# Optimization experiments

Hardware: AMD Instinct MI355X
Metric: run time of the kernel (lower is better)

Reference implementation:

```python
import jax, jax.numpy as jnp
import numpy as np

TEMP = 0.05          # self.temp
NUM_LABELED = 15080  # SysuDataset bank size


def setup_inputs() -> dict:
    key = jax.random.key(0)
    k1, k2, k3, k4, k5 = jax.random.split(key, 5)
    B, D, L = 512, 2048, NUM_LABELED
    f = jax.random.normal(k1, (B, D), jnp.float32)
    features = f / jnp.linalg.norm(f, axis=1, keepdims=True)  # L2-normalized embeddings
    fk = jax.random.normal(k2, (B, D), jnp.float32)
    features_k = fk / jnp.linalg.norm(fk, axis=1, keepdims=True)
    gt_labels = jax.random.randint(k3, (B, 5), 0, L)   # last column = pid index
    gt_labels_k = jax.random.randint(k4, (B, 5), 0, L)
    bank = jax.random.normal(k5, (L, D), jnp.float32)
    bank_features = bank / jnp.linalg.norm(bank, axis=1, keepdims=True)
    return {"features": features, "features_k": features_k,
            "gt_labels": gt_labels, "gt_labels_k": gt_labels_k,
            "bank_features": bank_features}


def reference(features, features_k, gt_labels, gt_labels_k, bank_features):
    # pids = cat([i[:, -1] for i in gt_labels]); all >= 0 by construction, so the
    # pids > -1 filter is an identity (static shapes under jit).
    pids = gt_labels[:, -1]                                  # [B]
    # HM.forward: inputs.mm(features.t()), then /= temp
    sim_all = (features @ bank_features.T) / TEMP            # [B, L]
    # segment-mean of logits grouped by memory label (labels == arange -> identity,
    # kept for faithfulness to the index_add / nums normalization in the source)
    labels = jnp.arange(NUM_LABELED)
    sim = jax.ops.segment_sum(sim_all.T, labels, num_segments=NUM_LABELED)  # [L, B]
    nums = jax.ops.segment_sum(jnp.ones((NUM_LABELED, 1), jnp.float32),
                               labels, num_segments=NUM_LABELED)            # [L, 1]
    sim = sim / nums
    logits = sim.T                                           # [B, L]
    logp = jax.nn.log_softmax(logits, axis=-1)
    loss = -jnp.mean(jnp.take_along_axis(logp, pids[:, None], axis=1))
    return loss
```

## Files before the change

kernel.cpp:

```cpp
#include <hip/hip_runtime.h>
#include <hip/hip_bf16.h>

#define M_ROWS 512
#define N_COLS 15080
#define K_DIM  2048
#define BM 128
#define BN 128
#define BKF 64
#define NT 118
#define KSTEPS 32
#define SCALE 20.0f

#define BANK_PAD_ROWS 15104
#define BANK_PAD_E (30932992ull)
#define FEAT_E     (1048576ull)
#define NG_CVT     (3997696ull)

typedef _Float16 f16x8 __attribute__((ext_vector_type(8)));
typedef float    f32x4 __attribute__((ext_vector_type(4)));

#define GLD_LDS16(gp, lp) __builtin_amdgcn_global_load_lds( \
    (const __attribute__((address_space(1))) void*)(gp),    \
    (__attribute__((address_space(3))) void*)(lp), 16, 0, 0)

extern "C" __global__ __launch_bounds__(256)
void k_cvt(const float* __restrict__ feat, const float* __restrict__ bank,
           _Float16* __restrict__ out)
{
    const size_t stride = (size_t)gridDim.x * 256;
    for (size_t g = (size_t)blockIdx.x * 256 + threadIdx.x; g < NG_CVT; g += stride) {
        const size_t e = g * 8;
        f16x8 h;
        if (e < BANK_PAD_E) {
            const int row = (int)(e >> 11);
            if (row < N_COLS) {
                const float4 x = *(const float4*)(bank + e);
                const float4 y = *(const float4*)(bank + e + 4);
                h[0] = (_Float16)x.x; h[1] = (_Float16)x.y; h[2] = (_Float16)x.z; h[3] = (_Float16)x.w;
                h[4] = (_Float16)y.x; h[5] = (_Float16)y.y; h[6] = (_Float16)y.z; h[7] = (_Float16)y.w;
            } else {
                h = (f16x8)(_Float16)0.0f;
            }
        } else {
            const size_t e2 = e - BANK_PAD_E;
            const float4 x = *(const float4*)(feat + e2);
            const float4 y = *(const float4*)(feat + e2 + 4);
            h[0] = (_Float16)x.x; h[1] = (_Float16)x.y; h[2] = (_Float16)x.z; h[3] = (_Float16)x.w;
            h[4] = (_Float16)y.x; h[5] = (_Float16)y.y; h[6] = (_Float16)y.z; h[7] = (_Float16)y.w;
        }
        *(f16x8*)(out + e) = h;
    }
}

extern "C" __global__ __launch_bounds__(256, 2)
void k_gemm16(const _Float16* __restrict__ A16,
              const _Float16* __restrict__ B16,
              const int*      __restrict__ gt,
              float* __restrict__ pm,
              float* __restrict__ ps,
              float* __restrict__ tv)
{
    __shared__ __align__(16) char lds[65536];

    const int t  = threadIdx.x;
    const int bx = blockIdx.x;

    int mi, nt;
    if (bx < 448) { const int slot = bx & 7; const int rest = bx >> 3;
                    mi = rest & 3; nt = (rest >> 2) * 8 + slot; }
    else          { const int r2 = bx - 448; mi = r2 & 3; nt = 112 + (r2 >> 2); }
    const int rowA0 = mi * BM;
    const int rowB0 = nt * BN;

    const int lane = t & 63, w = t >> 6;
    const int lr = lane >> 3, gg = lane & 7;
    const size_t aE0 = (size_t)(rowA0 + w * 32 + lr) * K_DIM + (size_t)((gg ^ lr) * 8);
    const size_t bE0 = (size_t)(rowB0 + w * 32 + lr) * K_DIM + (size_t)((gg ^ lr) * 8);
    const char* aP0 = (const char*)(A16 + aE0);
    const char* bP0 = (const char*)(B16 + bE0);
    const int ldsW = w * 4096;

    auto STAGE = [&](int kt, int sel) {
        const int   dofs = sel * 32768;
        const size_t ko  = (size_t)kt * 128;
#pragma unroll
        for (int j = 0; j < 4; j++) {
            GLD_LDS16(aP0 + (size_t)j * 32768 + ko, lds + dofs + ldsW + j * 1024);
            GLD_LDS16(bP0 + (size_t)j * 32768 + ko, lds + dofs + 16384 + ldsW + j * 1024);
        }
    };

    const int wm = w >> 1, wn = w & 1;
    const int q = lane >> 4, r = lane & 15;
    int aaddr[4][2], baddr[4][2];
#pragma unroll
    for (int m = 0; m < 4; m++) {
        const int rowa = wm * 64 + m * 16 + r;
        const int rowb = wn * 64 + m * 16 + r;
#pragma unroll
        for (int ks = 0; ks < 2; ks++) {
            aaddr[m][ks] = (rowa * 128 + ks * 64 + q * 16) ^ ((rowa & 7) << 4);
            baddr[m][ks] = 16384 + ((rowb * 128 + ks * 64 + q * 16) ^ ((rowb & 7) << 4));
        }
    }

    f32x4 acc[4][4];
    const f32x4 zero = {0.f, 0.f, 0.f, 0.f};
#pragma unroll
    for (int m = 0; m < 4; m++)
#pragma unroll
        for (int n = 0; n < 4; n++) acc[m][n] = zero;

    auto COMPUTE = [&](int sel) {
        const char* bb = lds + sel * 32768;
        f16x8 bf[4][2];
#pragma unroll
        for (int n = 0; n < 4; n++)
#pragma unroll
            for (int ks = 0; ks < 2; ks++)
                bf[n][ks] = *(const f16x8*)(bb + baddr[n][ks]);
#pragma unroll
        for (int m = 0; m < 4; m++) {
            const f16x8 af0 = *(const f16x8*)(bb + aaddr[m][0]);
            const f16x8 af1 = *(const f16x8*)(bb + aaddr[m][1]);
#pragma unroll
            for (int n = 0; n < 4; n++) {
                acc[m][n] = __builtin_amdgcn_mfma_f32_16x16x32_f16(af0, bf[n][0], acc[m][n], 0, 0, 0);
                acc[m][n] = __builtin_amdgcn_mfma_f32_16x16x32_f16(af1, bf[n][1], acc[m][n], 0, 0, 0);
            }
        }
    };

    STAGE(0, 0);
    __syncthreads();
#pragma unroll 2
    for (int kt = 0; kt < KSTEPS - 1; kt++) {
        STAGE(kt + 1, (kt + 1) & 1);
        COMPUTE(kt & 1);
        __syncthreads();
    }
    COMPUTE((KSTEPS - 1) & 1);

    __syncthreads();
    float* redm = (float*)lds;
    float* reds = ((float*)lds) + 256;

#pragma unroll
    for (int m = 0; m < 4; m++) {
#pragma unroll
        for (int j = 0; j < 4; j++) {
            const int lrow = wm * 64 + m * 16 + q * 4 + j;
            const int grow = rowA0 + lrow;
            const int pid  = gt[grow * 5 + 4];
            float sv[4];
            float mx = -INFINITY;
#pragma unroll
            for (int n = 0; n < 4; n++) {
                const int gc = rowB0 + wn * 64 + n * 16 + r;
                float s = SCALE * acc[m][n][j];
                s = (gc < N_COLS) ? s : -INFINITY;
                sv[n] = s;
                mx = fmaxf(mx, s);
                if (gc == pid) tv[grow] = s;
            }
#pragma unroll
            for (int d = 1; d < 16; d <<= 1) mx = fmaxf(mx, __shfl_xor(mx, d, 16));
            float se = 0.f;
#pragma unroll
            for (int n = 0; n < 4; n++) se += __expf(sv[n] - mx);
#pragma unroll
            for (int d = 1; d < 16; d <<= 1) se += __shfl_xor(se, d, 16);
            if (r == 0) { redm[wn * 128 + lrow] = mx; reds[wn * 128 + lrow] = se; }
        }
    }
    __syncthreads();
    if (t < 128) {
        const float m0 = redm[t], m1 = redm[128 + t];
        const float s0 = reds[t], s1 = reds[128 + t];
        const float Mv = fmaxf(m0, m1);
        const float Sv = s0 * __expf(m0 - Mv) + s1 * __expf(m1 - Mv);
        pm[(rowA0 + t) * NT + nt] = Mv;
        ps[(rowA0 + t) * NT + nt] = Sv;
    }
}

extern "C" __global__ __launch_bounds__(128)
void k_rowlse(const float* __restrict__ pm,
              const float* __restrict__ ps,
              const float* __restrict__ tv,
              float* __restrict__ rowloss)
{
    const int b = blockIdx.x;
    const int i = threadIdx.x;
    __shared__ float wred[4];

    const float m = (i < NT) ? pm[b * NT + i] : -INFINITY;
    const float s = (i < NT) ? ps[b * NT + i] : 0.f;

    float M = m;
#pragma unroll
    for (int d = 1; d < 64; d <<= 1) M = fmaxf(M, __shfl_xor(M, d, 64));
    if ((i & 63) == 0) wred[i >> 6] = M;
    __syncthreads();
    M = fmaxf(wred[0], wred[1]);
    __syncthreads();

    float e = (i < NT) ? s * __expf(m - M) : 0.f;
#pragma unroll
    for (int d = 1; d < 64; d <<= 1) e += __shfl_xor(e, d, 64);
    if ((i & 63) == 0) wred[i >> 6] = e;
    __syncthreads();
    if (i == 0) {
        const float S = wred[0] + wred[1];
        rowloss[b] = M + logf(S) - tv[b];
    }
}

extern "C" __global__ __launch_bounds__(512)
void k_final(const float* __restrict__ rowloss, float* __restrict__ out)
{
    __shared__ float red[512];
    const int b = threadIdx.x;
    red[b] = rowloss[b];
    __syncthreads();
    for (int s = 256; s > 0; s >>= 1) {
        if (b < s) red[b] += red[b + s];
        __syncthreads();
    }
    if (b == 0) out[0] = red[0] / 512.0f;
}

extern "C" __global__ __launch_bounds__(512, 4)
void k_gemm_lse(const float* __restrict__ A,
                const float* __restrict__ Bk,
                const int*   __restrict__ gt,
                float* __restrict__ pm, float* __restrict__ ps,
                float* __restrict__ tv)
{
    __shared__ __align__(16) ushort lds[16384];
    const int t  = threadIdx.x;
    const int bx = blockIdx.x;
    int mi, nt;
    if (bx < 448) { const int slot = bx & 7; const int rest = bx >> 3;
                    mi = rest & 3; nt = (rest >> 2) * 8 + slot; }
    else          { const int r2 = bx - 448; mi = r2 & 3; nt = 112 + (r2 >> 2); }
    const int rowA0 = mi * BM, rowB0 = nt * BN;

    int arow[2], ag[2];
#pragma unroll
    for (int i = 0; i < 2; i++) { int G = t + i * 512; arow[i] = G >> 3; ag[i] = G & 7; }
    float4 ra[4], rb[4];
    auto LOAD = [&](int kt) {
#pragma unroll
        for (int i = 0; i < 2; i++) {
            const float* pa = A + (size_t)(rowA0 + arow[i]) * K_DIM + kt * BKF + ag[i] * 8;
            ra[2*i] = *(const float4*)(pa); ra[2*i+1] = *(const float4*)(pa + 4);
            const int br = rowB0 + arow[i];
            if (br < N_COLS) {
                const float* pb = Bk + (size_t)br * K_DIM + kt * BKF + ag[i] * 8;
                rb[2*i] = *(const float4*)(pb); rb[2*i+1] = *(const float4*)(pb + 4);
            } else { rb[2*i] = make_float4(0,0,0,0); rb[2*i+1] = make_float4(0,0,0,0); }
        }
    };
    auto STORE = [&]() {
#pragma unroll
        for (int i = 0; i < 2; i++) {
            const int ba = (arow[i] * 128 + ag[i] * 16) ^ ((arow[i] & 7) << 4);
            f16x8 ha, hb;
            float4 x = ra[2*i], y = ra[2*i+1];
            ha[0]=(_Float16)x.x; ha[1]=(_Float16)x.y; ha[2]=(_Float16)x.z; ha[3]=(_Float16)x.w;
            ha[4]=(_Float16)y.x; ha[5]=(_Float16)y.y; ha[6]=(_Float16)y.z; ha[7]=(_Float16)y.w;
            x = rb[2*i]; y = rb[2*i+1];
            hb[0]=(_Float16)x.x; hb[1]=(_Float16)x.y; hb[2]=(_Float16)x.z; hb[3]=(_Float16)x.w;
            hb[4]=(_Float16)y.x; hb[5]=(_Float16)y.y; hb[6]=(_Float16)y.z; hb[7]=(_Float16)y.w;
            *(f16x8*)((char*)lds + ba) = ha;
            *(f16x8*)((char*)lds + 16384 + ba) = hb;
        }
    };
    const int lane = t & 63, wid = t >> 6;
    const int wm = wid >> 2, wn = wid & 3;
    const int q = lane >> 4, r = lane & 15;
    int aaddr[4][2], baddr[2][2];
#pragma unroll
    for (int m = 0; m < 4; m++) { const int rowa = wm*64 + m*16 + r;
#pragma unroll
        for (int ks = 0; ks < 2; ks++) aaddr[m][ks] = (rowa*128 + ks*64 + q*16) ^ ((rowa&7)<<4); }
#pragma unroll
    for (int n = 0; n < 2; n++) { const int rowb = wn*32 + n*16 + r;
#pragma unroll
        for (int ks = 0; ks < 2; ks++) baddr[n][ks] = 16384 + ((rowb*128 + ks*64 + q*16) ^ ((rowb&7)<<4)); }

    f32x4 acc[4][2];
    const f32x4 zero = {0.f,0.f,0.f,0.f};
#pragma unroll
    for (int m = 0; m < 4; m++)
#pragma unroll
        for (int n = 0; n < 2; n++) acc[m][n] = zero;

    LOAD(0);
    for (int kt = 0; kt < KSTEPS; kt++) {
        __syncthreads(); STORE(); __syncthreads();
        if (kt + 1 < KSTEPS) LOAD(kt + 1);
        f16x8 bf[2][2];
#pragma unroll
        for (int n = 0; n < 2; n++)
#pragma unroll
            for (int ks = 0; ks < 2; ks++) bf[n][ks] = *(const f16x8*)((const char*)lds + baddr[n][ks]);
#pragma unroll
        for (int m = 0; m < 4; m++) {
            const f16x8 af0 = *(const f16x8*)((const char*)lds + aaddr[m][0]);
            const f16x8 af1 = *(const f16x8*)((const char*)lds + aaddr[m][1]);
#pragma unroll
            for (int n = 0; n < 2; n++) {
                acc[m][n] = __builtin_amdgcn_mfma_f32_16x16x32_f16(af0, bf[n][0], acc[m][n], 0,0,0);
                acc[m][n] = __builtin_amdgcn_mfma_f32_16x16x32_f16(af1, bf[n][1], acc[m][n], 0,0,0);
            }
        }
    }
    __syncthreads();
    float* redm = (float*)lds;
    float* reds = ((float*)lds) + 512;
#pragma unroll
    for (int m = 0; m < 4; m++) {
#pragma unroll
        for (int j = 0; j < 4; j++) {
            const int lrow = wm*64 + m*16 + q*4 + j;
            const int grow = rowA0 + lrow;
            const int pid  = gt[grow*5 + 4];
            float sv[2]; float mx = -INFINITY;
#pragma unroll
            for (int n = 0; n < 2; n++) {
                const int gc = rowB0 + wn*32 + n*16 + r;
                float s = SCALE * acc[m][n][j];
                s = (gc < N_COLS) ? s : -INFINITY;
                sv[n] = s; mx = fmaxf(mx, s);
                if (gc == pid) tv[grow] = s;
            }
#pragma unroll
            for (int d = 1; d < 16; d <<= 1) mx = fmaxf(mx, __shfl_xor(mx, d, 16));
            float se = 0.f;
#pragma unroll
            for (int n = 0; n < 2; n++) se += __expf(sv[n] - mx);
#pragma unroll
            for (int d = 1; d < 16; d <<= 1) se += __shfl_xor(se, d, 16);
            if (r == 0) { redm[wn*128 + lrow] = mx; reds[wn*128 + lrow] = se; }
        }
    }
    __syncthreads();
    if (t < 128) {
        float Mv = -INFINITY;
#pragma unroll
        for (int c = 0; c < 4; c++) Mv = fmaxf(Mv, redm[c*128 + t]);
        float Sv = 0.f;
#pragma unroll
        for (int c = 0; c < 4; c++) Sv += reds[c*128 + t] * __expf(redm[c*128 + t] - Mv);
        pm[(rowA0 + t) * NT + nt] = Mv;
        ps[(rowA0 + t) * NT + nt] = Sv;
    }
}

extern "C" void kernel_launch(void* const* d_in, const int* in_sizes, int n_in,
                              void* d_out, int out_size, void* d_ws, size_t ws_size,
                              hipStream_t stream)
{
    const float* feat = (const float*)d_in[0];
    const int*   gt   = (const int*)d_in[2];
    const float* bank = (const float*)d_in[4];

    const size_t NEED = (BANK_PAD_E + FEAT_E) * 2 + (size_t)512 * NT * 4 * 2 + 512 * 4 * 2;
    if (ws_size >= NEED) {
        _Float16* bank16 = (_Float16*)d_ws;
        _Float16* feat16 = bank16 + BANK_PAD_E;
        float* pm = (float*)(feat16 + FEAT_E);
        float* ps = pm + 512 * NT;
        float* tv = ps + 512 * NT;
        float* rl = tv + 512;
        k_cvt<<<dim3(2048), 256, 0, stream>>>(feat, bank, bank16);
        k_gemm16<<<dim3(4 * NT), 256, 0, stream>>>(feat16, bank16, gt, pm, ps, tv);
        k_rowlse<<<dim3(512), 128, 0, stream>>>(pm, ps, tv, rl);
        k_final<<<dim3(1), 512, 0, stream>>>(rl, (float*)d_out);
    } else {
        float* pm = (float*)d_ws;
        float* ps = pm + 512 * NT;
        float* tv = ps + 512 * NT;
        float* rl = tv + 512;
        k_gemm_lse<<<dim3(4 * NT), 512, 0, stream>>>(feat, bank, gt, pm, ps, tv);
        k_rowlse<<<dim3(512), 128, 0, stream>>>(pm, ps, tv, rl);
        k_final<<<dim3(1), 512, 0, stream>>>(rl, (float*)d_out);
    }
}
```

Baseline: 239.5 us.

## Deepen GEMM LDS pipeline to four stages with explicit vmcnt waits

Replaces the double-buffered global-to-LDS pipeline with a 4-slot ring buffer in dynamic shared memory (128 KB), prefetching three k-steps ahead. The blanket __syncthreads is replaced by counted s_waitcnt vmcnt plus s_barrier, so loads stay in flight across iterations and memory latency is hidden better. Launch bounds drop to one block per CU because of the larger LDS footprint, which trades occupancy for deeper prefetch. The hand-written wait counts must match the number of outstanding loads per stage or correctness breaks.

```diff
diff --git a/kernel.cpp b/kernel.cpp
--- a/kernel.cpp
+++ b/kernel.cpp
@@ -52,7 +52,7 @@
     }
 }
 
-extern "C" __global__ __launch_bounds__(256, 2)
+extern "C" __global__ __launch_bounds__(256, 1)
 void k_gemm16(const _Float16* __restrict__ A16,
               const _Float16* __restrict__ B16,
               const int*      __restrict__ gt,
@@ -60,7 +60,7 @@
               float* __restrict__ ps,
               float* __restrict__ tv)
 {
-    __shared__ __align__(16) char lds[65536];
+    extern __shared__ char lds[];
 
     const int t  = threadIdx.x;
     const int bx = blockIdx.x;
@@ -80,8 +80,8 @@
     const char* bP0 = (const char*)(B16 + bE0);
     const int ldsW = w * 4096;
 
-    auto STAGE = [&](int kt, int sel) {
-        const int   dofs = sel * 32768;
+    auto STAGE = [&](int kt) {
+        const int   dofs = (kt & 3) * 32768;
         const size_t ko  = (size_t)kt * 128;
 #pragma unroll
         for (int j = 0; j < 4; j++) {
@@ -111,8 +111,8 @@
 #pragma unroll
         for (int n = 0; n < 4; n++) acc[m][n] = zero;
 
-    auto COMPUTE = [&](int sel) {
-        const char* bb = lds + sel * 32768;
+    auto COMPUTE = [&](int kt) {
+        const char* bb = lds + (kt & 3) * 32768;
         f16x8 bf[4][2];
 #pragma unroll
         for (int n = 0; n < 4; n++)
@@ -131,15 +131,20 @@
         }
     };
 
-    STAGE(0, 0);
-    __syncthreads();
-#pragma unroll 2
-    for (int kt = 0; kt < KSTEPS - 1; kt++) {
-        STAGE(kt + 1, (kt + 1) & 1);
-        COMPUTE(kt & 1);
-        __syncthreads();
-    }
-    COMPUTE((KSTEPS - 1) & 1);
+    STAGE(0); STAGE(1); STAGE(2);
+    asm volatile("s_waitcnt vmcnt(16)" ::: "memory");
+    __builtin_amdgcn_s_barrier();
+
+    for (int kt = 0; kt < KSTEPS; kt++) {
+        if (kt + 3 < KSTEPS) STAGE(kt + 3);
+        COMPUTE(kt);
+        if (kt + 1 < KSTEPS) {
+            if (kt <= KSTEPS - 4)      asm volatile("s_waitcnt vmcnt(16)" ::: "memory");
+            else if (kt == KSTEPS - 3) asm volatile("s_waitcnt vmcnt(8)"  ::: "memory");
+            else                       asm volatile("s_waitcnt vmcnt(0)"  ::: "memory");
+            __builtin_amdgcn_s_barrier();
+        }
+    }
 
     __syncthreads();
     float* redm = (float*)lds;
@@ -376,7 +381,7 @@
         float* tv = ps + 512 * NT;
         float* rl = tv + 512;
         k_cvt<<<dim3(2048), 256, 0, stream>>>(feat, bank, bank16);
-        k_gemm16<<<dim3(4 * NT), 256, 0, stream>>>(feat16, bank16, gt, pm, ps, tv);
+        k_gemm16<<<dim3(4 * NT), 256, 131072, stream>>>(feat16, bank16, gt, pm, ps, tv);
         k_rowlse<<<dim3(512), 128, 0, stream>>>(pm, ps, tv, rl);
         k_final<<<dim3(1), 512, 0, stream>>>(rl, (float*)d_out);
     } else {
```

Result: slower. 258.6 us (+8.0%).

## Split-K the fp16 GEMM in two and move the softmax reduction to a separate pass

Applied to the files above, without the earlier changes.

The fp16 MFMA GEMM now splits K into two halves, doubling the workgroup count from 472 to 944 so more waves are in flight across the CUs. Each half writes its raw partial dot products to a full [2, 512, N_PAD] fp32 workspace, with an XCD-aware block remap. A new per-row kernel sums the two partials, scales them, and computes an online log-sum-exp plus the target logit. This replaces the fused in-epilogue max/sum reduction. In exchange it adds roughly 62 MB of extra global writes and reads for the partial logits.

```diff
diff --git a/kernel.cpp b/kernel.cpp
--- a/kernel.cpp
+++ b/kernel.cpp
@@ -3,15 +3,18 @@
 
 #define M_ROWS 512
 #define N_COLS 15080
+#define N_PAD  15104
 #define K_DIM  2048
 #define BM 128
 #define BN 128
-#define BKF 64
 #define NT 118
 #define KSTEPS 32
 #define SCALE 20.0f
 
-#define BANK_PAD_ROWS 15104
+#define KS 2
+#define KSLICE 1024
+#define KSTEPS_SK 16
+
 #define BANK_PAD_E (30932992ull)
 #define FEAT_E     (1048576ull)
 #define NG_CVT     (3997696ull)
@@ -53,29 +56,28 @@
 }
 
 extern "C" __global__ __launch_bounds__(256, 2)
-void k_gemm16(const _Float16* __restrict__ A16,
-              const _Float16* __restrict__ B16,
-              const int*      __restrict__ gt,
-              float* __restrict__ pm,
-              float* __restrict__ ps,
-              float* __restrict__ tv)
+void k_gemm16sk(const _Float16* __restrict__ A16,
+                const _Float16* __restrict__ B16,
+                float* __restrict__ part)
 {
     __shared__ __align__(16) char lds[65536];
 
     const int t  = threadIdx.x;
     const int bx = blockIdx.x;
 
-    int mi, nt;
-    if (bx < 448) { const int slot = bx & 7; const int rest = bx >> 3;
-                    mi = rest & 3; nt = (rest >> 2) * 8 + slot; }
-    else          { const int r2 = bx - 448; mi = r2 & 3; nt = 112 + (r2 >> 2); }
+    const int wgid = (bx & 7) * 118 + (bx >> 3);
+    const int mi = wgid & 3;
+    const int ks = (wgid >> 2) & 1;
+    const int nt = wgid >> 3;
     const int rowA0 = mi * BM;
     const int rowB0 = nt * BN;
+    float* outp = part + (size_t)ks * M_ROWS * N_PAD;
 
     const int lane = t & 63, w = t >> 6;
     const int lr = lane >> 3, gg = lane & 7;
-    const size_t aE0 = (size_t)(rowA0 + w * 32 + lr) * K_DIM + (size_t)((gg ^ lr) * 8);
-    const size_t bE0 = (size_t)(rowB0 + w * 32 + lr) * K_DIM + (size_t)((gg ^ lr) * 8);
+    const size_t kbase = (size_t)ks * KSLICE;
+    const size_t aE0 = (size_t)(rowA0 + w * 32 + lr) * K_DIM + kbase + (size_t)((gg ^ lr) * 8);
+    const size_t bE0 = (size_t)(rowB0 + w * 32 + lr) * K_DIM + kbase + (size_t)((gg ^ lr) * 8);
     const char* aP0 = (const char*)(A16 + aE0);
     const char* bP0 = (const char*)(B16 + bE0);
     const int ldsW = w * 4096;
@@ -98,9 +100,9 @@
         const int rowa = wm * 64 + m * 16 + r;
         const int rowb = wn * 64 + m * 16 + r;
 #pragma unroll
-        for (int ks = 0; ks < 2; ks++) {
-            aaddr[m][ks] = (rowa * 128 + ks * 64 + q * 16) ^ ((rowa & 7) << 4);
-            baddr[m][ks] = 16384 + ((rowb * 128 + ks * 64 + q * 16) ^ ((rowb & 7) << 4));
+        for (int k2 = 0; k2 < 2; k2++) {
+            aaddr[m][k2] = (rowa * 128 + k2 * 64 + q * 16) ^ ((rowa & 7) << 4);
+            baddr[m][k2] = 16384 + ((rowb * 128 + k2 * 64 + q * 16) ^ ((rowb & 7) << 4));
         }
     }
 
@@ -117,8 +119,8 @@
 #pragma unroll
         for (int n = 0; n < 4; n++)
 #pragma unroll
-            for (int ks = 0; ks < 2; ks++)
-                bf[n][ks] = *(const f16x8*)(bb + baddr[n][ks]);
+            for (int k2 = 0; k2 < 2; k2++)
+                bf[n][k2] = *(const f16x8*)(bb + baddr[n][k2]);
 #pragma unroll
         for (int m = 0; m < 4; m++) {
             const f16x8 af0 = *(const f16x8*)(bb + aaddr[m][0]);
@@ -134,85 +136,66 @@
     STAGE(0, 0);
     __syncthreads();
 #pragma unroll 2
-    for (int kt = 0; kt < KSTEPS - 1; kt++) {
+    for (int kt = 0; kt < KSTEPS_SK - 1; kt++) {
         STAGE(kt + 1, (kt + 1) & 1);
         COMPUTE(kt & 1);
         __syncthreads();
     }
-    COMPUTE((KSTEPS - 1) & 1);
-
-    __syncthreads();
-    float* redm = (float*)lds;
-    float* reds = ((float*)lds) + 256;
-
-#pragma unroll
-    for (int m = 0; m < 4; m++) {
+    COMPUTE((KSTEPS_SK - 1) & 1);
+
+#pragma unroll
+    for (int m = 0; m < 4; m++)
 #pragma unroll
         for (int j = 0; j < 4; j++) {
-            const int lrow = wm * 64 + m * 16 + q * 4 + j;
-            const int grow = rowA0 + lrow;
-            const int pid  = gt[grow * 5 + 4];
-            float sv[4];
-            float mx = -INFINITY;
-#pragma unroll
-            for (int n = 0; n < 4; n++) {
-                const int gc = rowB0 + wn * 64 + n * 16 + r;
-                float s = SCALE * acc[m][n][j];
-                s = (gc < N_COLS) ? s : -INFINITY;
-                sv[n] = s;
-                mx = fmaxf(mx, s);
-                if (gc == pid) tv[grow] = s;
-            }
-#pragma unroll
-            for (int d = 1; d < 16; d <<= 1) mx = fmaxf(mx, __shfl_xor(mx, d, 16));
-            float se = 0.f;
-#pragma unroll
-            for (int n = 0; n < 4; n++) se += __expf(sv[n] - mx);
-#pragma unroll
-            for (int d = 1; d < 16; d <<= 1) se += __shfl_xor(se, d, 16);
-            if (r == 0) { redm[wn * 128 + lrow] = mx; reds[wn * 128 + lrow] = se; }
-        }
-    }
-    __syncthreads();
-    if (t < 128) {
-        const float m0 = redm[t], m1 = redm[128 + t];
-        const float s0 = reds[t], s1 = reds[128 + t];
-        const float Mv = fmaxf(m0, m1);
-        const float Sv = s0 * __expf(m0 - Mv) + s1 * __expf(m1 - Mv);
-        pm[(rowA0 + t) * NT + nt] = Mv;
-        ps[(rowA0 + t) * NT + nt] = Sv;
-    }
-}
-
-extern "C" __global__ __launch_bounds__(128)
-void k_rowlse(const float* __restrict__ pm,
-              const float* __restrict__ ps,
-              const float* __restrict__ tv,
-              float* __restrict__ rowloss)
+            const int grow = rowA0 + wm * 64 + m * 16 + q * 4 + j;
+            float* rowp = outp + (size_t)grow * N_PAD + rowB0 + wn * 64 + r;
+#pragma unroll
+            for (int n = 0; n < 4; n++) rowp[n * 16] = acc[m][n][j];
+        }
+}
+
+extern "C" __global__ __launch_bounds__(256)
+void k_lse(const float* __restrict__ part,
+           const int*   __restrict__ gt,
+           float* __restrict__ rowloss)
 {
     const int b = blockIdx.x;
-    const int i = threadIdx.x;
-    __shared__ float wred[4];
-
-    const float m = (i < NT) ? pm[b * NT + i] : -INFINITY;
-    const float s = (i < NT) ? ps[b * NT + i] : 0.f;
-
-    float M = m;
-#pragma unroll
-    for (int d = 1; d < 64; d <<= 1) M = fmaxf(M, __shfl_xor(M, d, 64));
-    if ((i & 63) == 0) wred[i >> 6] = M;
-    __syncthreads();
-    M = fmaxf(wred[0], wred[1]);
-    __syncthreads();
-
-    float e = (i < NT) ? s * __expf(m - M) : 0.f;
-#pragma unroll
-    for (int d = 1; d < 64; d <<= 1) e += __shfl_xor(e, d, 64);
-    if ((i & 63) == 0) wred[i >> 6] = e;
-    __syncthreads();
-    if (i == 0) {
-        const float S = wred[0] + wred[1];
-        rowloss[b] = M + logf(S) - tv[b];
+    const int t = threadIdx.x;
+    __shared__ float lm[4], ls[4];
+
+    const float4* p0 = (const float4*)(part + (size_t)b * N_PAD);
+    const float4* p1 = (const float4*)(part + (size_t)(M_ROWS + b) * N_PAD);
+
+    float m = -1e30f, s = 0.f;
+    for (int c = t; c < 3770; c += 256) {
+        const float4 a = p0[c], d = p1[c];
+        const float x0 = SCALE * (a.x + d.x);
+        const float x1 = SCALE * (a.y + d.y);
+        const float x2 = SCALE * (a.z + d.z);
+        const float x3 = SCALE * (a.w + d.w);
+        const float mx = fmaxf(fmaxf(x0, x1), fmaxf(x2, x3));
+        if (mx > m) { s *= __expf(m - mx); m = mx; }
+        s += __expf(x0 - m) + __expf(x1 - m) + __expf(x2 - m) + __expf(x3 - m);
+    }
+#pragma unroll
+    for (int d = 1; d < 64; d <<= 1) {
+        const float om = __shfl_xor(m, d, 64);
+        const float os = __shfl_xor(s, d, 64);
+        const float nm = fmaxf(m, om);
+        s = s * __expf(m - nm) + os * __expf(om - nm);
+        m = nm;
+    }
+    if ((t & 63) == 0) { lm[t >> 6] = m; ls[t >> 6] = s; }
+    __syncthreads();
+    if (t == 0) {
+        float M = fmaxf(fmaxf(lm[0], lm[1]), fmaxf(lm[2], lm[3]));
+        float S = 0.f;
+#pragma unroll
+        for (int w = 0; w < 4; w++) S += ls[w] * __expf(lm[w] - M);
+        const int pid = gt[b * 5 + 4];
+        const float tgt = SCALE * (part[(size_t)b * N_PAD + pid] +
+                                   part[(size_t)(M_ROWS + b) * N_PAD + pid]);
+        rowloss[b] = M + logf(S) - tgt;
     }
 }
 
@@ -253,11 +236,11 @@
     auto LOAD = [&](int kt) {
 #pragma unroll
         for (int i = 0; i < 2; i++) {
-            const float* pa = A + (size_t)(rowA0 + arow[i]) * K_DIM + kt * BKF + ag[i] * 8;
+            const float* pa = A + (size_t)(rowA0 + arow[i]) * K_DIM + kt * 64 + ag[i] * 8;
             ra[2*i] = *(const float4*)(pa); ra[2*i+1] = *(const float4*)(pa + 4);
             const int br = rowB0 + arow[i];
             if (br < N_COLS) {
-                const float* pb = Bk + (size_t)br * K_DIM + kt * BKF + ag[i] * 8;
+                const float* pb = Bk + (size_t)br * K_DIM + kt * 64 + ag[i] * 8;
                 rb[2*i] = *(const float4*)(pb); rb[2*i+1] = *(const float4*)(pb + 4);
             } else { rb[2*i] = make_float4(0,0,0,0); rb[2*i+1] = make_float4(0,0,0,0); }
         }
@@ -284,11 +267,11 @@
 #pragma unroll
     for (int m = 0; m < 4; m++) { const int rowa = wm*64 + m*16 + r;
 #pragma unroll
-        for (int ks = 0; ks < 2; ks++) aaddr[m][ks] = (rowa*128 + ks*64 + q*16) ^ ((rowa&7)<<4); }
+        for (int k2 = 0; k2 < 2; k2++) aaddr[m][k2] = (rowa*128 + k2*64 + q*16) ^ ((rowa&7)<<4); }
 #pragma unroll
     for (int n = 0; n < 2; n++) { const int rowb = wn*32 + n*16 + r;
 #pragma unroll
-        for (int ks = 0; ks < 2; ks++) baddr[n][ks] = 16384 + ((rowb*128 + ks*64 + q*16) ^ ((rowb&7)<<4)); }
+        for (int k2 = 0; k2 < 2; k2++) baddr[n][k2] = 16384 + ((rowb*128 + k2*64 + q*16) ^ ((rowb&7)<<4)); }
 
     f32x4 acc[4][2];
     const f32x4 zero = {0.f,0.f,0.f,0.f};
@@ -305,7 +288,7 @@
 #pragma unroll
         for (int n = 0; n < 2; n++)
 #pragma unroll
-            for (int ks = 0; ks < 2; ks++) bf[n][ks] = *(const f16x8*)((const char*)lds + baddr[n][ks]);
+            for (int k2 = 0; k2 < 2; k2++) bf[n][k2] = *(const f16x8*)((const char*)lds + baddr[n][k2]);
 #pragma unroll
         for (int m = 0; m < 4; m++) {
             const f16x8 af0 = *(const f16x8*)((const char*)lds + aaddr[m][0]);
@@ -359,6 +342,38 @@
     }
 }
 
+extern "C" __global__ __launch_bounds__(128)
+void k_rowlse(const float* __restrict__ pm,
+              const float* __restrict__ ps,
+              const float* __restrict__ tv,
+              float* __restrict__ rowloss)
+{
+    const int b = blockIdx.x;
+    const int i = threadIdx.x;
+    __shared__ float wred[4];
+
+    const float m = (i < NT) ? pm[b * NT + i] : -INFINITY;
+    const float s = (i < NT) ? ps[b * NT + i] : 0.f;
+
+    float M = m;
+#pragma unroll
+    for (int d = 1; d < 64; d <<= 1) M = fmaxf(M, __shfl_xor(M, d, 64));
+    if ((i & 63) == 0) wred[i >> 6] = M;
+    __syncthreads();
+    M = fmaxf(wred[0], wred[1]);
+    __syncthreads();
+
+    float e = (i < NT) ? s * __expf(m - M) : 0.f;
+#pragma unroll
+    for (int d = 1; d < 64; d <<= 1) e += __shfl_xor(e, d, 64);
+    if ((i & 63) == 0) wred[i >> 6] = e;
+    __syncthreads();
+    if (i == 0) {
+        const float S = wred[0] + wred[1];
+        rowloss[b] = M + logf(S) - tv[b];
+    }
+}
+
 extern "C" void kernel_launch(void* const* d_in, const int* in_sizes, int n_in,
                               void* d_out, int out_size, void* d_ws, size_t ws_size,
                               hipStream_t stream)
@@ -367,17 +382,16 @@
     const int*   gt   = (const int*)d_in[2];
     const float* bank = (const float*)d_in[4];
 
-    const size_t NEED = (BANK_PAD_E + FEAT_E) * 2 + (size_t)512 * NT * 4 * 2 + 512 * 4 * 2;
+    const size_t NEED = (BANK_PAD_E + FEAT_E) * 2
+                      + (size_t)KS * M_ROWS * N_PAD * 4 + 512 * 4;
     if (ws_size >= NEED) {
         _Float16* bank16 = (_Float16*)d_ws;
         _Float16* feat16 = bank16 + BANK_PAD_E;
-        float* pm = (float*)(feat16 + FEAT_E);
-        float* ps = pm + 512 * NT;
-        float* tv = ps + 512 * NT;
-        float* rl = tv + 512;
+        float* part = (float*)(feat16 + FEAT_E);
+        float* rl   = part + (size_t)KS * M_ROWS * N_PAD;
         k_cvt<<<dim3(2048), 256, 0, stream>>>(feat, bank, bank16);
-        k_gemm16<<<dim3(4 * NT), 256, 0, stream>>>(feat16, bank16, gt, pm, ps, tv);
-        k_rowlse<<<dim3(512), 128, 0, stream>>>(pm, ps, tv, rl);
+        k_gemm16sk<<<dim3(8 * NT), 256, 0, stream>>>(feat16, bank16, part);
+        k_lse<<<dim3(M_ROWS), 256, 0, stream>>>(part, gt, rl);
         k_final<<<dim3(1), 512, 0, stream>>>(rl, (float*)d_out);
     } else {
         float* pm = (float*)d_ws;
```

New measurement: 246.2 us. +2.8%, slower.
